# Kernel tuning notes

Measured on AMD Instinct MI355X. Metric: run time of the kernel, lower is better.

The kernel has to match this reference:

```python
import jax, jax.numpy as jnp
import numpy as np

HEADS = 8
UNITS = 1024
D_ATT = UNITS // HEADS  # 128
NEG_INF = -1e9  # matches Keras Attention additive causal mask


def setup_inputs() -> dict:
    key = jax.random.key(0)
    kx, kq, kk, kv, ko = jax.random.split(key, 5)
    B, T = 4, 2048
    scale = 0.02
    x = jax.random.normal(kx, (B, T, UNITS), dtype=jnp.float32)
    Wq = jax.random.normal(kq, (UNITS, HEADS * D_ATT), dtype=jnp.float32) * scale
    Wk = jax.random.normal(kk, (UNITS, HEADS * D_ATT), dtype=jnp.float32) * scale
    Wv = jax.random.normal(kv, (UNITS, D_ATT), dtype=jnp.float32) * scale
    Wo = jax.random.normal(ko, (D_ATT, UNITS), dtype=jnp.float32) * scale
    return {"x": x, "Wq": Wq, "Wk": Wk, "Wv": Wv, "Wo": Wo}


def reference(x, Wq, Wk, Wv, Wo):
    # TFT interpretable multi-head self-attention (inference; dropout inactive).
    B, T, U = x.shape
    H, d = HEADS, D_ATT
    scale = 1.0 / jnp.sqrt(jnp.asarray(d, x.dtype))  # query / sqrt(shape(key)[-1])
    q = (x @ Wq).reshape(B, T, H, d) * scale          # [B,T,H,d]
    k = (x @ Wk).reshape(B, T, H, d)                  # [B,T,H,d]
    v = x @ Wv                                        # [B,T,d], shared across heads
    scores = jnp.einsum("bthd,bshd->bhts", q, k)      # [B,H,T,T]
    causal = jnp.tril(jnp.ones((T, T), dtype=bool))   # [T,T]
    scores = jnp.where(causal, scores, jnp.asarray(NEG_INF, scores.dtype))
    w = jax.nn.softmax(scores, axis=-1)               # [B,H,T,T]
    out = jnp.einsum("bhts,bsd->bthd", w, v)          # [B,T,H,d]
    out = out.mean(axis=2) @ Wo                       # mean over heads -> Dense(units)
    attn = w.mean(axis=1)                             # mean attention over heads [B,T,T]
    return out, attn
```

## Files before the change

kernel.cpp:

```cpp
#include <hip/hip_runtime.h>

#define BATCH 4
#define TSEQ  2048
#define UNITS 1024
#define HEADS 8
#define DH    128
#define MROWS (BATCH*TSEQ)
#define NCAT  (2*UNITS + DH)

typedef short bf16x8 __attribute__((ext_vector_type(8)));
typedef short short4v __attribute__((ext_vector_type(4)));
typedef float f32x4  __attribute__((ext_vector_type(4)));

__device__ __forceinline__ short f2bf(float f){
    union { float f; unsigned u; } v; v.f = f;
    unsigned r = v.u + 0x7fff + ((v.u >> 16) & 1);
    return (short)(r >> 16);
}
__device__ __forceinline__ float redsum16(float v){
    #pragma unroll
    for (int m = 1; m < 16; m <<= 1) v += __shfl_xor(v, m);
    return v;
}
__device__ __forceinline__ void gload_lds16(const void* g, void* l){
    __builtin_amdgcn_global_load_lds(
        (const __attribute__((address_space(1))) void*)g,
        (__attribute__((address_space(3))) void*)l, 16, 0, 0);
}

#define SWZB(r, cbyte) ((cbyte) ^ (((r) & 7) << 4))

#define QSCALE (0.08838834764831845f * 1.4426950408889634f)

__global__ __launch_bounds__(256) void xcast_kernel(const float* __restrict__ x,
                                                    short* __restrict__ Xbf)
{
    const int N = MROWS*UNITS/8;
    for (int i = blockIdx.x*256 + threadIdx.x; i < N; i += gridDim.x*256){
        f32x4 a = *(const f32x4*)(x + (size_t)i*8);
        f32x4 b = *(const f32x4*)(x + (size_t)i*8 + 4);
        bf16x8 o;
        o[0]=f2bf(a[0]); o[1]=f2bf(a[1]); o[2]=f2bf(a[2]); o[3]=f2bf(a[3]);
        o[4]=f2bf(b[0]); o[5]=f2bf(b[1]); o[6]=f2bf(b[2]); o[7]=f2bf(b[3]);
        *(bf16x8*)(Xbf + (size_t)i*8) = o;
    }
}

__global__ __launch_bounds__(256) void wtrans_kernel(
    const float* __restrict__ Wq, const float* __restrict__ Wk,
    const float* __restrict__ Wv, const float* __restrict__ Wo,
    short* __restrict__ WT, short* __restrict__ WoT)
{
    __shared__ float T_lds[64][65];
    const int tid = threadIdx.x;
    const int bid = blockIdx.x;
    if (bid < 544){
        const int nt = bid >> 4, kt = bid & 15;
        const int n0 = nt*64, k0 = kt*64;
        const float* src; int scol; float sc = 1.0f; int sstride = UNITS;
        if (n0 < UNITS){ src = Wq; scol = n0; sc = QSCALE; }
        else if (n0 < 2*UNITS){ src = Wk; scol = n0 - UNITS; }
        else { src = Wv; scol = n0 - 2*UNITS; sstride = DH; }
        const int ln = tid & 63, lk0 = tid >> 6;
        for (int kk = lk0; kk < 64; kk += 4)
            T_lds[kk][ln] = src[(size_t)(k0+kk)*sstride + scol + ln] * sc;
        __syncthreads();
        const int lk = tid & 63, ln0 = tid >> 6;
        for (int nn = ln0; nn < 64; nn += 4)
            WT[(size_t)(n0+nn)*UNITS + k0 + lk] = f2bf(T_lds[lk][nn]);
    } else {
        const int t = bid - 544;
        const int nt = t >> 1, dt = t & 1;
        const int n0 = nt*64, d0 = dt*64;
        const int ln = tid & 63, lk0 = tid >> 6;
        for (int dd = lk0; dd < 64; dd += 4)
            T_lds[dd][ln] = Wo[(size_t)(d0+dd)*UNITS + n0 + ln];
        __syncthreads();
        const int ld = tid & 63, ln0 = tid >> 6;
        for (int nn = ln0; nn < 64; nn += 4)
            WoT[(size_t)(n0+nn)*DH + d0 + ld] = f2bf(T_lds[ld][nn]);
    }
}

__global__ __launch_bounds__(256) void gemm_qkv_kernel(
    const short* __restrict__ X, const short* __restrict__ WT,
    short* __restrict__ Qbf, short* __restrict__ Kbf, short* __restrict__ Vt)
{
    __shared__ short A_lds[128][32];
    __shared__ short B_lds[128][32];
    const int tid = threadIdx.x;
    const int w = tid >> 6, l = tid & 63, lg = l >> 4, lr = l & 15;
    const int wm = w >> 1, wn = w & 1;
    const int n0 = blockIdx.x * 128;
    const int m0 = blockIdx.y * 128;
    const f32x4 fzero = {0.f, 0.f, 0.f, 0.f};
    f32x4 acc[4][4];
    #pragma unroll
    for (int i = 0; i < 4; i++)
        #pragma unroll
        for (int j = 0; j < 4; j++) acc[i][j] = fzero;

    const int srow = (l >> 2);
    const int scol = (l & 3) * 8;

    for (int k0 = 0; k0 < UNITS; k0 += 32){
        #pragma unroll
        for (int i = 0; i < 2; i++){
            int row = w*32 + i*16 + srow;
            gload_lds16(X  + (size_t)(m0+row)*UNITS + k0 + scol,
                        (char*)A_lds + ((w*2 + i) << 10));
            gload_lds16(WT + (size_t)(n0+row)*UNITS + k0 + scol,
                        (char*)B_lds + ((w*2 + i) << 10));
        }
        __syncthreads();
        bf16x8 af[4], bfr[4];
        #pragma unroll
        for (int mf = 0; mf < 4; mf++)
            af[mf] = *(const bf16x8*)(&A_lds[wm*64 + mf*16 + lr][lg*8]);
        #pragma unroll
        for (int nf = 0; nf < 4; nf++)
            bfr[nf] = *(const bf16x8*)(&B_lds[wn*64 + nf*16 + lr][lg*8]);
        #pragma unroll
        for (int mf = 0; mf < 4; mf++)
            #pragma unroll
            for (int nf = 0; nf < 4; nf++)
                acc[mf][nf] = __builtin_amdgcn_mfma_f32_16x16x32_bf16(
                    af[mf], bfr[nf], acc[mf][nf], 0, 0, 0);
        __syncthreads();
    }

    #pragma unroll
    for (int mf = 0; mf < 4; mf++){
        #pragma unroll
        for (int nf = 0; nf < 4; nf++){
            #pragma unroll
            for (int r = 0; r < 4; r++){
                int gr = m0 + wm*64 + mf*16 + lg*4 + r;
                int gc = n0 + wn*64 + nf*16 + lr;
                int b = gr >> 11, t = gr & 2047;
                short v = f2bf(acc[mf][nf][r]);
                if (gc < UNITS){
                    int h = gc >> 7, dd = gc & 127;
                    Qbf[(((size_t)(b*HEADS + h))*TSEQ + t)*DH + dd] = v;
                } else if (gc < 2*UNITS){
                    int h = (gc - UNITS) >> 7, dd = gc & 127;
                    Kbf[(((size_t)(b*HEADS + h))*TSEQ + t)*DH + dd] = v;
                } else {
                    int dd = gc - 2*UNITS;
                    Vt[((size_t)b*DH + dd)*TSEQ + t] = v;
                }
            }
        }
    }
}

__global__ __launch_bounds__(256) void stats_kernel(
    const short* __restrict__ Qbf, const short* __restrict__ Kbf,
    float* __restrict__ Lb)
{
    __shared__ short K_lds[2][64][128];
    const int tid = threadIdx.x;
    const int w = tid >> 6, l = tid & 63, lg = l >> 4, lr = l & 15;
    const int bh = blockIdx.y;
    const int qt = 31 - blockIdx.x;
    const int q0 = qt * 64;
    const short* Qh = Qbf + (size_t)bh*TSEQ*DH;
    const short* Kh = Kbf + (size_t)bh*TSEQ*DH;
    const f32x4 fzero = {0.f, 0.f, 0.f, 0.f};

    const int srow = tid >> 4;
    const int sc8  = tid & 15;

    const int qrow = q0 + w*16 + lr;
    bf16x8 aq[4];
    #pragma unroll
    for (int ks = 0; ks < 4; ks++)
        aq[ks] = *(const bf16x8*)(Qh + (size_t)qrow*DH + ks*32 + lg*8);

    bf16x8 kreg[4];
    #pragma unroll
    for (int i = 0; i < 4; i++)
        kreg[i] = *(const bf16x8*)(Kh + (size_t)(srow + i*16)*DH + sc8*8);
    #pragma unroll
    for (int i = 0; i < 4; i++){
        int r = srow + i*16;
        *(bf16x8*)((char*)&K_lds[0][0][0] + r*256 + SWZB(r, sc8*16)) = kreg[i];
    }
    __syncthreads();

    float lrow[4] = {0.f, 0.f, 0.f, 0.f};
    const int ntile = qt + 1;
    for (int t = 0; t < ntile; t++){
        const int cur = t & 1;
        if (t + 1 < ntile){
            const size_t base = (size_t)((t+1)*64 + srow)*DH + sc8*8;
            #pragma unroll
            for (int i = 0; i < 4; i++)
                kreg[i] = *(const bf16x8*)(Kh + base + (size_t)i*16*DH);
        }
        f32x4 sacc[4];
        #pragma unroll
        for (int nf = 0; nf < 4; nf++) sacc[nf] = fzero;
        __builtin_amdgcn_s_setprio(1);
        #pragma unroll
        for (int ks = 0; ks < 4; ks++){
            #pragma unroll
            for (int nf = 0; nf < 4; nf++){
                int r = nf*16 + lr;
                bf16x8 kb = *(const bf16x8*)((char*)&K_lds[cur][0][0]
                              + r*256 + SWZB(r, ks*64 + lg*16));
                sacc[nf] = __builtin_amdgcn_mfma_f32_16x16x32_bf16(aq[ks], kb, sacc[nf], 0,0,0);
            }
        }
        __builtin_amdgcn_s_setprio(0);
        if (t == qt){
            #pragma unroll
            for (int nf = 0; nf < 4; nf++)
                #pragma unroll
                for (int r = 0; r < 4; r++)
                    if (nf*16 + lr > w*16 + lg*4 + r) sacc[nf][r] = -1e30f;
        }
        #pragma unroll
        for (int r = 0; r < 4; r++)
            lrow[r] += (exp2f(sacc[0][r]) + exp2f(sacc[1][r]))
                     + (exp2f(sacc[2][r]) + exp2f(sacc[3][r]));
        if (t + 1 < ntile){
            #pragma unroll
            for (int i = 0; i < 4; i++){
                int r = srow + i*16;
                *(bf16x8*)((char*)&K_lds[cur ^ 1][0][0] + r*256 + SWZB(r, sc8*16)) = kreg[i];
            }
        }
        __syncthreads();
    }
    #pragma unroll
    for (int r = 0; r < 4; r++) lrow[r] = redsum16(lrow[r]);
    if (lr == 0){
        #pragma unroll
        for (int r = 0; r < 4; r++){
            int t = q0 + w*16 + lg*4 + r;
            Lb[(size_t)bh*TSEQ + t] = 1.0f / lrow[r];
        }
    }
}

__global__ __launch_bounds__(256, 5) void attn_kernel(
    const short* __restrict__ Qbf, const short* __restrict__ Kbf,
    const float* __restrict__ Lb, float* __restrict__ attn)
{
    const int tid = threadIdx.x;
    const int b = blockIdx.y;
    const int qt = blockIdx.x >> 5, kvt = blockIdx.x & 31;
    const int q0 = qt*64, k0 = kvt*64;
    float* At = attn + (size_t)b*TSEQ*TSEQ;

    if (kvt > qt){
        const f32x4 fz = {0.f, 0.f, 0.f, 0.f};
        #pragma unroll
        for (int i = 0; i < 4; i++){
            int c = tid + i*256;
            int row = c >> 4, c4 = c & 15;
            *(f32x4*)(At + (size_t)(q0+row)*TSEQ + k0 + c4*4) = fz;
        }
        return;
    }

    __shared__ short K_lds[2][64][128];
    const int w = tid >> 6, l = tid & 63, lg = l >> 4, lr = l & 15;
    const int srow = tid >> 4, sc8 = tid & 15;
    const f32x4 fzero = {0.f, 0.f, 0.f, 0.f};
    const size_t bh0 = (size_t)(b*HEADS)*TSEQ*DH;

    bf16x8 kreg[4];
    {
        const short* Kh = Kbf + bh0;
        #pragma unroll
        for (int i = 0; i < 4; i++)
            kreg[i] = *(const bf16x8*)(Kh + (size_t)(k0 + srow + i*16)*DH + sc8*8);
        #pragma unroll
        for (int i = 0; i < 4; i++){
            int r = srow + i*16;
            *(bf16x8*)((char*)&K_lds[0][0][0] + r*256 + SWZB(r, sc8*16)) = kreg[i];
        }
    }
    bf16x8 aq[4];
    #pragma unroll
    for (int ks = 0; ks < 4; ks++)
        aq[ks] = *(const bf16x8*)(Qbf + bh0 + (size_t)(q0 + w*16 + lr)*DH + ks*32 + lg*8);
    __syncthreads();

    f32x4 wacc[4];
    #pragma unroll
    for (int nf = 0; nf < 4; nf++) wacc[nf] = fzero;

    for (int h = 0; h < HEADS; h++){
        const int cur = h & 1;
        bf16x8 aqn[4];
        if (h + 1 < HEADS){
            const size_t bhn = bh0 + (size_t)(h+1)*TSEQ*DH;
            const short* Kn = Kbf + bhn;
            #pragma unroll
            for (int i = 0; i < 4; i++)
                kreg[i] = *(const bf16x8*)(Kn + (size_t)(k0 + srow + i*16)*DH + sc8*8);
            const short* Qn = Qbf + bhn;
            #pragma unroll
            for (int ks = 0; ks < 4; ks++)
                aqn[ks] = *(const bf16x8*)(Qn + (size_t)(q0 + w*16 + lr)*DH + ks*32 + lg*8);
        }

        f32x4 sacc[4];
        #pragma unroll
        for (int nf = 0; nf < 4; nf++) sacc[nf] = fzero;
        __builtin_amdgcn_s_setprio(1);
        #pragma unroll
        for (int ks = 0; ks < 4; ks++){
            #pragma unroll
            for (int nf = 0; nf < 4; nf++){
                int r = nf*16 + lr;
                bf16x8 kb = *(const bf16x8*)((char*)&K_lds[cur][0][0]
                              + r*256 + SWZB(r, ks*64 + lg*16));
                sacc[nf] = __builtin_amdgcn_mfma_f32_16x16x32_bf16(aq[ks], kb, sacc[nf], 0,0,0);
            }
        }
        __builtin_amdgcn_s_setprio(0);

        if (kvt == qt){
            #pragma unroll
            for (int nf = 0; nf < 4; nf++)
                #pragma unroll
                for (int r = 0; r < 4; r++)
                    if (nf*16 + lr > w*16 + lg*4 + r) sacc[nf][r] = -1e30f;
        }
        f32x4 rlh = *(const f32x4*)(Lb + ((size_t)(b*HEADS + h))*TSEQ + q0 + w*16 + lg*4);
        #pragma unroll
        for (int nf = 0; nf < 4; nf++)
            #pragma unroll
            for (int r = 0; r < 4; r++)
                wacc[nf][r] += exp2f(sacc[nf][r]) * rlh[r];

        if (h + 1 < HEADS){
            #pragma unroll
            for (int i = 0; i < 4; i++){
                int r = srow + i*16;
                *(bf16x8*)((char*)&K_lds[cur ^ 1][0][0] + r*256 + SWZB(r, sc8*16)) = kreg[i];
            }
            #pragma unroll
            for (int ks = 0; ks < 4; ks++) aq[ks] = aqn[ks];
        }
        __syncthreads();
    }

    float* ob = (float*)&K_lds[0][0][0];
    #pragma unroll
    for (int nf = 0; nf < 4; nf++)
        #pragma unroll
        for (int r = 0; r < 4; r++)
            ob[(w*16 + lg*4 + r)*68 + nf*16 + lr] = wacc[nf][r] * 0.125f;
    __syncthreads();
    #pragma unroll
    for (int i = 0; i < 4; i++){
        int c = tid + i*256;
        int row = c >> 4, c4 = c & 15;
        *(f32x4*)(At + (size_t)(q0+row)*TSEQ + k0 + c4*4) =
            *(const f32x4*)(ob + row*68 + c4*4);
    }
}

__global__ __launch_bounds__(256) void pv_kernel(
    const float* __restrict__ attn, const short* __restrict__ Vt,
    float* __restrict__ Obuf)
{
    __shared__ short A_lds[64][72];
    __shared__ short V_lds[128][72];
    const int tid = threadIdx.x;
    const int w = tid >> 6, l = tid & 63, lg = l >> 4, lr = l & 15;
    const int mt = blockIdx.x;
    const int ks0 = blockIdx.y;
    const int b = blockIdx.z;
    const int m0 = mt*64;
    const int kmax = m0 + 64;
    const int kbeg = ks0*512;
    if (kbeg >= kmax) return;
    const int kend = min(kbeg + 512, kmax);
    const int nact = (kmax + 511) >> 9;
    const float* Ab = attn + (size_t)b*TSEQ*TSEQ;
    const short* Vb = Vt + (size_t)b*DH*TSEQ;
    const f32x4 fzero = {0.f, 0.f, 0.f, 0.f};
    f32x4 acc[8];
    #pragma unroll
    for (int i = 0; i < 8; i++) acc[i] = fzero;

    for (int k0 = kbeg; k0 < kend; k0 += 64){
        #pragma unroll
        for (int i = 0; i < 4; i++){
            int c = tid + i*256;
            int row = c >> 4, c4 = c & 15;
            f32x4 av = *(const f32x4*)(Ab + (size_t)(m0+row)*TSEQ + k0 + c4*4);
            short4v o;
            o[0]=f2bf(av[0]); o[1]=f2bf(av[1]); o[2]=f2bf(av[2]); o[3]=f2bf(av[3]);
            *(short4v*)(&A_lds[row][c4*4]) = o;
        }
        #pragma unroll
        for (int i = 0; i < 4; i++){
            int c = tid + i*256;
            int row = c >> 3, c8 = c & 7;
            *(bf16x8*)(&V_lds[row][c8*8]) =
                *(const bf16x8*)(Vb + (size_t)row*TSEQ + k0 + c8*8);
        }
        __syncthreads();
        __builtin_amdgcn_s_setprio(1);
        #pragma unroll
        for (int ks = 0; ks < 2; ks++){
            bf16x8 a = *(const bf16x8*)(&A_lds[w*16 + lr][ks*32 + lg*8]);
            #pragma unroll
            for (int cg = 0; cg < 8; cg++){
                bf16x8 vb = *(const bf16x8*)(&V_lds[cg*16 + lr][ks*32 + lg*8]);
                acc[cg] = __builtin_amdgcn_mfma_f32_16x16x32_bf16(a, vb, acc[cg], 0,0,0);
            }
        }
        __builtin_amdgcn_s_setprio(0);
        __syncthreads();
    }
    #pragma unroll
    for (int cg = 0; cg < 8; cg++)
        #pragma unroll
        for (int r = 0; r < 4; r++){
            int row = m0 + w*16 + lg*4 + r, col = cg*16 + lr;
            float* p = &Obuf[((size_t)b*TSEQ + row)*DH + col];
            if (nact == 1) *p = acc[cg][r];
            else atomicAdd(p, acc[cg][r]);
        }
}

__global__ __launch_bounds__(256) void gemm_out_kernel(
    const float* __restrict__ Ob, const short* __restrict__ WoT,
    float* __restrict__ out)
{
    __shared__ short A_lds[128][40];
    __shared__ short B_lds[128][40];
    const int tid = threadIdx.x;
    const int w = tid >> 6, l = tid & 63, lg = l >> 4, lr = l & 15;
    const int wm = w >> 1, wn = w & 1;
    const int n0 = blockIdx.x * 128;
    const int m0 = blockIdx.y * 128;
    const f32x4 fzero = {0.f, 0.f, 0.f, 0.f};
    f32x4 acc[4][4];
    #pragma unroll
    for (int i = 0; i < 4; i++)
        #pragma unroll
        for (int j = 0; j < 4; j++) acc[i][j] = fzero;

    for (int k0 = 0; k0 < DH; k0 += 32){
        #pragma unroll
        for (int i = 0; i < 2; i++){
            int c = tid + i*256;
            int row = c >> 2, c8 = c & 3;
            f32x4 a0 = *(const f32x4*)(Ob + (size_t)(m0+row)*DH + k0 + c8*8);
            f32x4 a1 = *(const f32x4*)(Ob + (size_t)(m0+row)*DH + k0 + c8*8 + 4);
            bf16x8 o;
            o[0]=f2bf(a0[0]); o[1]=f2bf(a0[1]); o[2]=f2bf(a0[2]); o[3]=f2bf(a0[3]);
            o[4]=f2bf(a1[0]); o[5]=f2bf(a1[1]); o[6]=f2bf(a1[2]); o[7]=f2bf(a1[3]);
            *(bf16x8*)(&A_lds[row][c8*8]) = o;
            *(bf16x8*)(&B_lds[row][c8*8]) =
                *(const bf16x8*)(WoT + (size_t)(n0+row)*DH + k0 + c8*8);
        }
        __syncthreads();
        bf16x8 af[4], bfr[4];
        #pragma unroll
        for (int mf = 0; mf < 4; mf++)
            af[mf] = *(const bf16x8*)(&A_lds[wm*64 + mf*16 + lr][lg*8]);
        #pragma unroll
        for (int nf = 0; nf < 4; nf++)
            bfr[nf] = *(const bf16x8*)(&B_lds[wn*64 + nf*16 + lr][lg*8]);
        #pragma unroll
        for (int mf = 0; mf < 4; mf++)
            #pragma unroll
            for (int nf = 0; nf < 4; nf++)
                acc[mf][nf] = __builtin_amdgcn_mfma_f32_16x16x32_bf16(
                    af[mf], bfr[nf], acc[mf][nf], 0, 0, 0);
        __syncthreads();
    }
    #pragma unroll
    for (int mf = 0; mf < 4; mf++)
        #pragma unroll
        for (int nf = 0; nf < 4; nf++)
            #pragma unroll
            for (int r = 0; r < 4; r++){
                int gr = m0 + wm*64 + mf*16 + lg*4 + r;
                int gc = n0 + wn*64 + nf*16 + lr;
                out[(size_t)gr*UNITS + gc] = acc[mf][nf][r];
            }
}

extern "C" void kernel_launch(void* const* d_in, const int* in_sizes, int n_in,
                              void* d_out, int out_size, void* d_ws, size_t ws_size,
                              hipStream_t stream)
{
    const float* x  = (const float*)d_in[0];
    const float* Wq = (const float*)d_in[1];
    const float* Wk = (const float*)d_in[2];
    const float* Wv = (const float*)d_in[3];
    const float* Wo = (const float*)d_in[4];
    float* out  = (float*)d_out;
    float* attn = out + (size_t)MROWS*UNITS;

    char* ws = (char*)d_ws;
    short* Xbf = (short*)(ws);
    short* WT  = (short*)(ws + 16777216);
    short* Qbf = (short*)(ws + 21233664);
    short* Kbf = (short*)(ws + 38010880);
    short* Vt  = (short*)(ws + 54788096);
    float* Lb  = (float*)(ws + 57147392);
    short* WoT = (short*)(ws + 57409536);
    float* Obuf = (float*)ws;

    xcast_kernel<<<2048, 256, 0, stream>>>(x, Xbf);
    wtrans_kernel<<<576, 256, 0, stream>>>(Wq, Wk, Wv, Wo, WT, WoT);
    gemm_qkv_kernel<<<dim3(NCAT/128, MROWS/128), 256, 0, stream>>>(Xbf, WT, Qbf, Kbf, Vt);
    hipMemsetAsync(Obuf, 0, (size_t)MROWS*DH*sizeof(float), stream);
    stats_kernel<<<dim3(TSEQ/64, BATCH*HEADS), 256, 0, stream>>>(Qbf, Kbf, Lb);
    attn_kernel<<<dim3(32*32, BATCH), 256, 0, stream>>>(Qbf, Kbf, Lb, attn);
    pv_kernel<<<dim3(TSEQ/64, 4, BATCH), 256, 0, stream>>>(attn, Vt, Obuf);
    gemm_out_kernel<<<dim3(UNITS/128, MROWS/128), 256, 0, stream>>>(Obuf, WoT, out);
}
```

Baseline: 376.1 us.

## Use 2x2 wave tiling in stats and attn kernels to halve LDS K reads

Changes the per-wave work split in stats_kernel and attn_kernel from 16 query rows by 64 keys to 32 query rows by 32 keys. Each K fragment read from LDS now feeds two MFMAs, which halves LDS read traffic per wave. Stats adds a cross-wave LDS reduction of the row sums, and attn moves the next-head Q prefetch after the MFMA loop to reuse the aq registers. Launch-bounds occupancy hints drop to 4 blocks per CU because of higher register pressure, and attn loses some load-latency hiding for Q.

```diff
diff --git a/kernel.cpp b/kernel.cpp
--- a/kernel.cpp
+++ b/kernel.cpp
@@ -154,13 +154,14 @@
     }
 }
 
-__global__ __launch_bounds__(256) void stats_kernel(
+__global__ __launch_bounds__(256, 4) void stats_kernel(
     const short* __restrict__ Qbf, const short* __restrict__ Kbf,
     float* __restrict__ Lb)
 {
     __shared__ short K_lds[2][64][128];
     const int tid = threadIdx.x;
     const int w = tid >> 6, l = tid & 63, lg = l >> 4, lr = l & 15;
+    const int wq = w >> 1, wk = w & 1;
     const int bh = blockIdx.y;
     const int qt = 31 - blockIdx.x;
     const int q0 = qt * 64;
@@ -171,11 +172,12 @@
     const int srow = tid >> 4;
     const int sc8  = tid & 15;
 
-    const int qrow = q0 + w*16 + lr;
-    bf16x8 aq[4];
-    #pragma unroll
-    for (int ks = 0; ks < 4; ks++)
-        aq[ks] = *(const bf16x8*)(Qh + (size_t)qrow*DH + ks*32 + lg*8);
+    bf16x8 aq[2][4];
+    #pragma unroll
+    for (int qf = 0; qf < 2; qf++)
+        #pragma unroll
+        for (int ks = 0; ks < 4; ks++)
+            aq[qf][ks] = *(const bf16x8*)(Qh + (size_t)(q0 + wq*32 + qf*16 + lr)*DH + ks*32 + lg*8);
 
     bf16x8 kreg[4];
     #pragma unroll
@@ -188,7 +190,7 @@
     }
     __syncthreads();
 
-    float lrow[4] = {0.f, 0.f, 0.f, 0.f};
+    float lrow[2][4] = {};
     const int ntile = qt + 1;
     for (int t = 0; t < ntile; t++){
         const int cur = t & 1;
@@ -198,32 +200,39 @@
             for (int i = 0; i < 4; i++)
                 kreg[i] = *(const bf16x8*)(Kh + base + (size_t)i*16*DH);
         }
-        f32x4 sacc[4];
-        #pragma unroll
-        for (int nf = 0; nf < 4; nf++) sacc[nf] = fzero;
+        f32x4 sacc[2][2];
+        #pragma unroll
+        for (int qf = 0; qf < 2; qf++)
+            #pragma unroll
+            for (int nf = 0; nf < 2; nf++) sacc[qf][nf] = fzero;
         __builtin_amdgcn_s_setprio(1);
         #pragma unroll
         for (int ks = 0; ks < 4; ks++){
             #pragma unroll
-            for (int nf = 0; nf < 4; nf++){
-                int r = nf*16 + lr;
+            for (int nf = 0; nf < 2; nf++){
+                int r = wk*32 + nf*16 + lr;
                 bf16x8 kb = *(const bf16x8*)((char*)&K_lds[cur][0][0]
                               + r*256 + SWZB(r, ks*64 + lg*16));
-                sacc[nf] = __builtin_amdgcn_mfma_f32_16x16x32_bf16(aq[ks], kb, sacc[nf], 0,0,0);
+                sacc[0][nf] = __builtin_amdgcn_mfma_f32_16x16x32_bf16(aq[0][ks], kb, sacc[0][nf], 0,0,0);
+                sacc[1][nf] = __builtin_amdgcn_mfma_f32_16x16x32_bf16(aq[1][ks], kb, sacc[1][nf], 0,0,0);
             }
         }
         __builtin_amdgcn_s_setprio(0);
         if (t == qt){
             #pragma unroll
-            for (int nf = 0; nf < 4; nf++)
+            for (int qf = 0; qf < 2; qf++)
                 #pragma unroll
-                for (int r = 0; r < 4; r++)
-                    if (nf*16 + lr > w*16 + lg*4 + r) sacc[nf][r] = -1e30f;
-        }
-        #pragma unroll
-        for (int r = 0; r < 4; r++)
-            lrow[r] += (exp2f(sacc[0][r]) + exp2f(sacc[1][r]))
-                     + (exp2f(sacc[2][r]) + exp2f(sacc[3][r]));
+                for (int nf = 0; nf < 2; nf++)
+                    #pragma unroll
+                    for (int r = 0; r < 4; r++)
+                        if (wk*32 + nf*16 + lr > wq*32 + qf*16 + lg*4 + r)
+                            sacc[qf][nf][r] = -1e30f;
+        }
+        #pragma unroll
+        for (int qf = 0; qf < 2; qf++)
+            #pragma unroll
+            for (int r = 0; r < 4; r++)
+                lrow[qf][r] += exp2f(sacc[qf][0][r]) + exp2f(sacc[qf][1][r]);
         if (t + 1 < ntile){
             #pragma unroll
             for (int i = 0; i < 4; i++){
@@ -234,17 +243,23 @@
         __syncthreads();
     }
     #pragma unroll
-    for (int r = 0; r < 4; r++) lrow[r] = redsum16(lrow[r]);
+    for (int qf = 0; qf < 2; qf++)
+        #pragma unroll
+        for (int r = 0; r < 4; r++) lrow[qf][r] = redsum16(lrow[qf][r]);
+    float* ps = (float*)&K_lds[0][0][0];
     if (lr == 0){
         #pragma unroll
-        for (int r = 0; r < 4; r++){
-            int t = q0 + w*16 + lg*4 + r;
-            Lb[(size_t)bh*TSEQ + t] = 1.0f / lrow[r];
-        }
-    }
-}
-
-__global__ __launch_bounds__(256, 5) void attn_kernel(
+        for (int qf = 0; qf < 2; qf++)
+            #pragma unroll
+            for (int r = 0; r < 4; r++)
+                ps[wk*64 + wq*32 + qf*16 + lg*4 + r] = lrow[qf][r];
+    }
+    __syncthreads();
+    if (tid < 64)
+        Lb[(size_t)bh*TSEQ + q0 + tid] = 1.0f / (ps[tid] + ps[64 + tid]);
+}
+
+__global__ __launch_bounds__(256, 4) void attn_kernel(
     const short* __restrict__ Qbf, const short* __restrict__ Kbf,
     const float* __restrict__ Lb, float* __restrict__ attn)
 {
@@ -267,6 +282,7 @@
 
     __shared__ short K_lds[2][64][128];
     const int w = tid >> 6, l = tid & 63, lg = l >> 4, lr = l & 15;
+    const int wq = w >> 1, wk = w & 1;
     const int srow = tid >> 4, sc8 = tid & 15;
     const f32x4 fzero = {0.f, 0.f, 0.f, 0.f};
     const size_t bh0 = (size_t)(b*HEADS)*TSEQ*DH;
@@ -283,60 +299,77 @@
             *(bf16x8*)((char*)&K_lds[0][0][0] + r*256 + SWZB(r, sc8*16)) = kreg[i];
         }
     }
-    bf16x8 aq[4];
-    #pragma unroll
-    for (int ks = 0; ks < 4; ks++)
-        aq[ks] = *(const bf16x8*)(Qbf + bh0 + (size_t)(q0 + w*16 + lr)*DH + ks*32 + lg*8);
+    bf16x8 aq[2][4];
+    #pragma unroll
+    for (int qf = 0; qf < 2; qf++)
+        #pragma unroll
+        for (int ks = 0; ks < 4; ks++)
+            aq[qf][ks] = *(const bf16x8*)(Qbf + bh0 + (size_t)(q0 + wq*32 + qf*16 + lr)*DH + ks*32 + lg*8);
     __syncthreads();
 
-    f32x4 wacc[4];
-    #pragma unroll
-    for (int nf = 0; nf < 4; nf++) wacc[nf] = fzero;
+    f32x4 wacc[2][2];
+    #pragma unroll
+    for (int qf = 0; qf < 2; qf++)
+        #pragma unroll
+        for (int nf = 0; nf < 2; nf++) wacc[qf][nf] = fzero;
 
     for (int h = 0; h < HEADS; h++){
         const int cur = h & 1;
-        bf16x8 aqn[4];
         if (h + 1 < HEADS){
-            const size_t bhn = bh0 + (size_t)(h+1)*TSEQ*DH;
-            const short* Kn = Kbf + bhn;
+            const short* Kn = Kbf + bh0 + (size_t)(h+1)*TSEQ*DH;
             #pragma unroll
             for (int i = 0; i < 4; i++)
                 kreg[i] = *(const bf16x8*)(Kn + (size_t)(k0 + srow + i*16)*DH + sc8*8);
-            const short* Qn = Qbf + bhn;
-            #pragma unroll
-            for (int ks = 0; ks < 4; ks++)
-                aqn[ks] = *(const bf16x8*)(Qn + (size_t)(q0 + w*16 + lr)*DH + ks*32 + lg*8);
-        }
-
-        f32x4 sacc[4];
-        #pragma unroll
-        for (int nf = 0; nf < 4; nf++) sacc[nf] = fzero;
+        }
+
+        f32x4 sacc[2][2];
+        #pragma unroll
+        for (int qf = 0; qf < 2; qf++)
+            #pragma unroll
+            for (int nf = 0; nf < 2; nf++) sacc[qf][nf] = fzero;
         __builtin_amdgcn_s_setprio(1);
         #pragma unroll
         for (int ks = 0; ks < 4; ks++){
             #pragma unroll
-            for (int nf = 0; nf < 4; nf++){
-                int r = nf*16 + lr;
+            for (int nf = 0; nf < 2; nf++){
+                int r = wk*32 + nf*16 + lr;
                 bf16x8 kb = *(const bf16x8*)((char*)&K_lds[cur][0][0]
                               + r*256 + SWZB(r, ks*64 + lg*16));
-                sacc[nf] = __builtin_amdgcn_mfma_f32_16x16x32_bf16(aq[ks], kb, sacc[nf], 0,0,0);
+                sacc[0][nf] = __builtin_amdgcn_mfma_f32_16x16x32_bf16(aq[0][ks], kb, sacc[0][nf], 0,0,0);
+                sacc[1][nf] = __builtin_amdgcn_mfma_f32_16x16x32_bf16(aq[1][ks], kb, sacc[1][nf], 0,0,0);
             }
         }
         __builtin_amdgcn_s_setprio(0);
 
+        if (h + 1 < HEADS){
+            const short* Qn = Qbf + bh0 + (size_t)(h+1)*TSEQ*DH;
+            #pragma unroll
+            for (int qf = 0; qf < 2; qf++)
+                #pragma unroll
+                for (int ks = 0; ks < 4; ks++)
+                    aq[qf][ks] = *(const bf16x8*)(Qn + (size_t)(q0 + wq*32 + qf*16 + lr)*DH + ks*32 + lg*8);
+        }
+
         if (kvt == qt){
             #pragma unroll
-            for (int nf = 0; nf < 4; nf++)
+            for (int qf = 0; qf < 2; qf++)
+                #pragma unroll
+                for (int nf = 0; nf < 2; nf++)
+                    #pragma unroll
+                    for (int r = 0; r < 4; r++)
+                        if (wk*32 + nf*16 + lr > wq*32 + qf*16 + lg*4 + r)
+                            sacc[qf][nf][r] = -1e30f;
+        }
+        const float* Lh = Lb + ((size_t)(b*HEADS + h))*TSEQ;
+        #pragma unroll
+        for (int qf = 0; qf < 2; qf++){
+            f32x4 rlh = *(const f32x4*)(Lh + q0 + wq*32 + qf*16 + lg*4);
+            #pragma unroll
+            for (int nf = 0; nf < 2; nf++)
                 #pragma unroll
                 for (int r = 0; r < 4; r++)
-                    if (nf*16 + lr > w*16 + lg*4 + r) sacc[nf][r] = -1e30f;
-        }
-        f32x4 rlh = *(const f32x4*)(Lb + ((size_t)(b*HEADS + h))*TSEQ + q0 + w*16 + lg*4);
-        #pragma unroll
-        for (int nf = 0; nf < 4; nf++)
-            #pragma unroll
-            for (int r = 0; r < 4; r++)
-                wacc[nf][r] += exp2f(sacc[nf][r]) * rlh[r];
+                    wacc[qf][nf][r] += exp2f(sacc[qf][nf][r]) * rlh[r];
+        }
 
         if (h + 1 < HEADS){
             #pragma unroll
@@ -344,18 +377,18 @@
                 int r = srow + i*16;
                 *(bf16x8*)((char*)&K_lds[cur ^ 1][0][0] + r*256 + SWZB(r, sc8*16)) = kreg[i];
             }
-            #pragma unroll
-            for (int ks = 0; ks < 4; ks++) aq[ks] = aqn[ks];
         }
         __syncthreads();
     }
 
     float* ob = (float*)&K_lds[0][0][0];
     #pragma unroll
-    for (int nf = 0; nf < 4; nf++)
-        #pragma unroll
-        for (int r = 0; r < 4; r++)
-            ob[(w*16 + lg*4 + r)*68 + nf*16 + lr] = wacc[nf][r] * 0.125f;
+    for (int qf = 0; qf < 2; qf++)
+        #pragma unroll
+        for (int nf = 0; nf < 2; nf++)
+            #pragma unroll
+            for (int r = 0; r < 4; r++)
+                ob[(wq*32 + qf*16 + lg*4 + r)*68 + wk*32 + nf*16 + lr] = wacc[qf][nf][r] * 0.125f;
     __syncthreads();
     #pragma unroll
     for (int i = 0; i < 4; i++){
```

New measurement: 803.2 us. +113.6%, slower.
